# Performance work log

Measured on AMD Instinct MI355X. Metric: run time of the kernel, lower is better.

The kernel has to match this reference:

```python
import jax, jax.numpy as jnp
import numpy as np

SZ = 3072
D = 1024
B, T = 4, 8192
VOCAB = 50257


def setup_inputs() -> dict:
    key = jax.random.key(0)
    k1, k2, k3 = jax.random.split(key, 3)
    t = jax.random.randint(k1, (B, T), 0, VOCAB, dtype=jnp.int32)
    tab = jax.random.normal(k2, (SZ, D), dtype=jnp.float32)
    w_proj = jax.random.normal(k3, (D, D), dtype=jnp.float32) / np.sqrt(D)
    return {"t": t, "tab": tab, "w_proj": w_proj}


def _hash_idx(t, sz):
    # prev token, padded with 0 at position 0
    prev = jnp.pad(t[:, :-1], ((0, 0), (1, 0)))
    # (t*31337 + prev*1000003) % sz, computed overflow-safely in int32
    # using modular arithmetic: (a*b) % m == ((a%m)*(b%m)) % m
    a = (t % sz) * (31337 % sz)
    b = (prev % sz) * (1000003 % sz)
    return (a + b) % sz


def reference(t, tab, w_proj):
    idx = _hash_idx(t, SZ)              # [B, T] in [0, SZ)
    emb = tab[idx]                      # [B, T, D] gather
    # F.linear(x, W) = x @ W.T
    return jnp.einsum('btd,ed->bte', emb, w_proj)
```

## Files before the change

kernel.cpp:

```cpp
#include <hip/hip_runtime.h>
#include <hip/hip_bf16.h>
#include <stdint.h>

#define SZ 3072
#define D_ 1024
#define BB 4
#define TT 8192
#define NROWS (BB * TT)

typedef unsigned short u16;
typedef __bf16 bf16x8 __attribute__((ext_vector_type(8)));
typedef float f32x4 __attribute__((ext_vector_type(4)));


__device__ __forceinline__ u16 f2bf(float f) {
    union { float f; uint32_t u; } c;
    c.f = f;
    uint32_t u = c.u;
    uint32_t r = (u + 0x7FFFu + ((u >> 16) & 1u)) >> 16;
    return (u16)r;
}

__device__ __forceinline__ void gload_lds16(const void* g, void* l) {
    __builtin_amdgcn_global_load_lds(
        (__attribute__((address_space(1))) void*)(void*)g,
        (__attribute__((address_space(3))) void*)l,
        16, 0, 0);
}

__device__ __forceinline__ int hash_pair(int cur, int prev) {
    int a = (cur % SZ) * (31337 % SZ);
    int b = (prev % SZ) * (1000003 % SZ);
    return (a + b) % SZ;
}


__global__ __launch_bounds__(256) void convert_kernel(
    const float* __restrict__ tab, const float* __restrict__ w,
    u16* __restrict__ tabb, u16* __restrict__ wb) {
    const int NT4 = SZ * D_ / 4;
    const int NTOT = NT4 + D_ * D_ / 4;
    int i = blockIdx.x * 256 + threadIdx.x;
    if (i >= NTOT) return;
    const float4* src;
    u16* dst;
    int o;
    if (i < NT4) { src = (const float4*)tab; dst = tabb; o = i; }
    else         { src = (const float4*)w;   dst = wb;   o = i - NT4; }
    float4 v = src[o];
    unsigned long long pack =
        (unsigned long long)f2bf(v.x) |
        ((unsigned long long)f2bf(v.y) << 16) |
        ((unsigned long long)f2bf(v.z) << 32) |
        ((unsigned long long)f2bf(v.w) << 48);
    *(unsigned long long*)&dst[o * 4] = pack;
}


__global__ __launch_bounds__(256) void gemm_p_kernel(
    const u16* __restrict__ Ab,
    const u16* __restrict__ Wb,
    float* __restrict__ P) {
    __shared__ __align__(16) u16 As[64][32];
    __shared__ __align__(16) u16 Ws[64][32];

    const int bid = blockIdx.x;
    const int wgid = (bid & 7) * 96 + (bid >> 3);
    const int brow = wgid >> 4;
    const int bcol = wgid & 15;
    const int row0 = brow << 6;
    const int col0 = bcol << 6;

    const int tid = threadIdx.x;
    const int lane = tid & 63;
    const int w = tid >> 6;
    const int wr = (w >> 1) << 5;
    const int wc = (w & 1) << 5;
    const int lrow = lane & 15;
    const int k8 = (lane >> 4) << 3;

    const int r0 = tid >> 2, kk0 = (tid & 3) << 3;

    f32x4 acc[2][2];
#pragma unroll
    for (int m = 0; m < 2; ++m)
#pragma unroll
        for (int n = 0; n < 2; ++n)
            acc[m][n] = f32x4{0.f, 0.f, 0.f, 0.f};

    for (int k0 = 0; k0 < D_; k0 += 32) {
        gload_lds16(&Ab[(row0 + r0) * D_ + k0 + kk0], &As[r0][kk0]);
        gload_lds16(&Wb[(col0 + r0) * D_ + k0 + kk0], &Ws[r0][kk0]);
        __syncthreads();

        bf16x8 av[2], bv[2];
#pragma unroll
        for (int m = 0; m < 2; ++m)
            av[m] = *(const bf16x8*)&As[wr + m * 16 + lrow][k8];
#pragma unroll
        for (int n = 0; n < 2; ++n)
            bv[n] = *(const bf16x8*)&Ws[wc + n * 16 + lrow][k8];
#pragma unroll
        for (int m = 0; m < 2; ++m)
#pragma unroll
            for (int n = 0; n < 2; ++n)
                acc[m][n] = __builtin_amdgcn_mfma_f32_16x16x32_bf16(
                    av[m], bv[n], acc[m][n], 0, 0, 0);
        __syncthreads();
    }

    const int rbase = (lane >> 4) << 2;
#pragma unroll
    for (int m = 0; m < 2; ++m)
#pragma unroll
        for (int n = 0; n < 2; ++n)
#pragma unroll
            for (int r = 0; r < 4; ++r)
                P[(row0 + wr + m * 16 + rbase + r) * D_ + col0 + wc + n * 16 + lrow] =
                    acc[m][n][r];
}


__global__ __launch_bounds__(256) void gather_kernel(
    const float* __restrict__ P, const int* __restrict__ t,
    float* __restrict__ out) {
    const int total = NROWS * (D_ / 4);
    const f32x4* P4 = (const f32x4*)P;
    f32x4* O4 = (f32x4*)out;
    for (int v = blockIdx.x * 256 + threadIdx.x; v < total; v += gridDim.x * 256) {
        int row = v >> 8;
        int c4 = v & 255;
        int cur = t[row];
        int prev = ((row & (TT - 1)) == 0) ? 0 : t[row - 1];
        int s = hash_pair(cur, prev);
        f32x4 val = P4[s * 256 + c4];
        __builtin_nontemporal_store(val, &O4[v]);
    }
}


__global__ __launch_bounds__(256) void fallback_kernel(
    const int* __restrict__ t, const float* __restrict__ tab,
    const float* __restrict__ w, float* __restrict__ out) {
    __shared__ float emb[D_];
    int row = blockIdx.x;
    int j = row & (TT - 1);
    int cur = t[row];
    int prev = (j == 0) ? 0 : t[row - 1];
    int s = hash_pair(cur, prev);
    for (int d = threadIdx.x; d < D_; d += 256) emb[d] = tab[s * D_ + d];
    __syncthreads();
    for (int e = threadIdx.x; e < D_; e += 256) {
        float accv = 0.f;
        const float* wrow = &w[e * D_];
        for (int d = 0; d < D_; ++d) accv += emb[d] * wrow[d];
        out[(size_t)row * D_ + e] = accv;
    }
}


extern "C" void kernel_launch(void* const* d_in, const int* in_sizes, int n_in,
                              void* d_out, int out_size, void* d_ws, size_t ws_size,
                              hipStream_t stream) {
    const int* t = (const int*)d_in[0];
    const float* tab = (const float*)d_in[1];
    const float* w = (const float*)d_in[2];
    float* out = (float*)d_out;

    const size_t off_tabb = 0;
    const size_t off_wb   = (size_t)SZ * D_ * 2;
    const size_t off_P    = off_wb + (size_t)D_ * D_ * 2;
    const size_t need     = off_P + (size_t)SZ * D_ * 4;

    if (ws_size < need) {
        fallback_kernel<<<NROWS, 256, 0, stream>>>(t, tab, w, out);
        return;
    }

    u16* tabb = (u16*)((char*)d_ws + off_tabb);
    u16* wb   = (u16*)((char*)d_ws + off_wb);
    float* P  = (float*)((char*)d_ws + off_P);

    convert_kernel<<<4096, 256, 0, stream>>>(tab, w, tabb, wb);
    gemm_p_kernel<<<(SZ / 64) * (D_ / 64), 256, 0, stream>>>(tabb, wb, P);
    gather_kernel<<<2048, 256, 0, stream>>>(P, t, out);
}
```

Measured before the change: 188.9 us.

## Fuse gather into GEMM epilogue via per-bucket row lists and scatter stores

New measurement: 201.7 us. 1.07x slower.

```diff
diff --git a/kernel.cpp b/kernel.cpp
--- a/kernel.cpp
+++ b/kernel.cpp
@@ -7,6 +7,7 @@
 #define BB 4
 #define TT 8192
 #define NROWS (BB * TT)
+#define CAP 128
 
 typedef unsigned short u16;
 typedef __bf16 bf16x8 __attribute__((ext_vector_type(8)));
@@ -57,12 +58,28 @@
 }
 
 
-__global__ __launch_bounds__(256) void gemm_p_kernel(
+__global__ __launch_bounds__(256) void bucket_kernel(
+    const int* __restrict__ t, int* __restrict__ count, int* __restrict__ lists) {
+    int i = blockIdx.x * 256 + threadIdx.x;
+    if (i >= NROWS) return;
+    int j = i & (TT - 1);
+    int cur = t[i];
+    int prev = (j == 0) ? 0 : t[i - 1];
+    int s = hash_pair(cur, prev);
+    int pos = atomicAdd(&count[s], 1);
+    if (pos < CAP) lists[s * CAP + pos] = i;
+}
+
+
+__global__ __launch_bounds__(256) void gemm_scatter_kernel(
     const u16* __restrict__ Ab,
     const u16* __restrict__ Wb,
-    float* __restrict__ P) {
+    const int* __restrict__ count,
+    const int* __restrict__ lists,
+    float* __restrict__ out) {
     __shared__ __align__(16) u16 As[64][32];
     __shared__ __align__(16) u16 Ws[64][32];
+    __shared__ __align__(16) float tile[64][68];
 
     const int bid = blockIdx.x;
     const int wgid = (bid & 7) * 96 + (bid >> 3);
@@ -116,25 +133,23 @@
         for (int n = 0; n < 2; ++n)
 #pragma unroll
             for (int r = 0; r < 4; ++r)
-                P[(row0 + wr + m * 16 + rbase + r) * D_ + col0 + wc + n * 16 + lrow] =
-                    acc[m][n][r];
-}
-
-
-__global__ __launch_bounds__(256) void gather_kernel(
-    const float* __restrict__ P, const int* __restrict__ t,
-    float* __restrict__ out) {
-    const int total = NROWS * (D_ / 4);
-    const f32x4* P4 = (const f32x4*)P;
-    f32x4* O4 = (f32x4*)out;
-    for (int v = blockIdx.x * 256 + threadIdx.x; v < total; v += gridDim.x * 256) {
-        int row = v >> 8;
-        int c4 = v & 255;
-        int cur = t[row];
-        int prev = ((row & (TT - 1)) == 0) ? 0 : t[row - 1];
-        int s = hash_pair(cur, prev);
-        f32x4 val = P4[s * 256 + c4];
-        __builtin_nontemporal_store(val, &O4[v]);
+                tile[wr + m * 16 + rbase + r][wc + n * 16 + lrow] = acc[m][n][r];
+    __syncthreads();
+
+    const int dup = tid >> 4;
+    const int c4 = (tid & 15) << 2;
+    for (int r = 0; r < 64; ++r) {
+        int s = row0 + r;
+        int cnt = count[s];
+        f32x4 val = *(const f32x4*)&tile[r][c4];
+        for (int base = 0; base < cnt; base += 16) {
+            int d = base + dup;
+            if (d < cnt) {
+                int orow = lists[s * CAP + d];
+                __builtin_nontemporal_store(
+                    val, (f32x4*)&out[(size_t)orow * D_ + col0 + c4]);
+            }
+        }
     }
 }
 
@@ -167,21 +182,25 @@
     const float* w = (const float*)d_in[2];
     float* out = (float*)d_out;
 
-    const size_t off_tabb = 0;
-    const size_t off_wb   = (size_t)SZ * D_ * 2;
-    const size_t off_P    = off_wb + (size_t)D_ * D_ * 2;
-    const size_t need     = off_P + (size_t)SZ * D_ * 4;
+    const size_t off_tabb  = 0;
+    const size_t off_wb    = (size_t)SZ * D_ * 2;
+    const size_t off_count = off_wb + (size_t)D_ * D_ * 2;
+    const size_t off_lists = off_count + (size_t)SZ * 4;
+    const size_t need      = off_lists + (size_t)SZ * CAP * 4;
 
     if (ws_size < need) {
         fallback_kernel<<<NROWS, 256, 0, stream>>>(t, tab, w, out);
         return;
     }
 
-    u16* tabb = (u16*)((char*)d_ws + off_tabb);
-    u16* wb   = (u16*)((char*)d_ws + off_wb);
-    float* P  = (float*)((char*)d_ws + off_P);
-
+    u16* tabb  = (u16*)((char*)d_ws + off_tabb);
+    u16* wb    = (u16*)((char*)d_ws + off_wb);
+    int* count = (int*)((char*)d_ws + off_count);
+    int* lists = (int*)((char*)d_ws + off_lists);
+
+    hipMemsetAsync(count, 0, (size_t)SZ * 4, stream);
     convert_kernel<<<4096, 256, 0, stream>>>(tab, w, tabb, wb);
-    gemm_p_kernel<<<(SZ / 64) * (D_ / 64), 256, 0, stream>>>(tabb, wb, P);
-    gather_kernel<<<2048, 256, 0, stream>>>(P, t, out);
-}
+    bucket_kernel<<<NROWS / 256, 256, 0, stream>>>(t, count, lists);
+    gemm_scatter_kernel<<<(SZ / 64) * (D_ / 64), 256, 0, stream>>>(
+        tabb, wb, count, lists, out);
+}
```
